# Performance work log

Hardware: AMD Instinct MI355X
Metric: run time of the kernel (lower is better)

The kernel has to match this reference:

```python
import jax, jax.numpy as jnp
import numpy as np

TOP_K_PCT = 0.1
MAX_SHARP_TOKENS = 10
SMOOTHING = 0.1


def setup_inputs() -> dict:
    key = jax.random.key(0)
    logits = jax.random.normal(key, (2, 8, 2048, 2048), dtype=jnp.float32)
    return {"logits": logits, "dim": 3}


def reference(logits, dim):
    # Move the softmax axis to the end so lax.top_k / row-scatter apply.
    x = jnp.moveaxis(logits, dim, -1)
    N = x.shape[-1]
    k = min(MAX_SHARP_TOKENS, max(1, int(N * TOP_K_PCT)))

    vals, idx = jax.lax.top_k(x, k)            # [..., k], sorted descending
    topk_soft = jax.nn.softmax(vals, axis=-1)  # softmax over just the top-k values

    flat = x.reshape(-1, N)                    # [R, N]
    fidx = idx.reshape(-1, k)                  # [R, k]
    rows = jnp.arange(flat.shape[0])[:, None]

    # boolean mask of top-k positions
    mask = jnp.zeros(flat.shape, dtype=bool).at[rows, fidx].set(True)

    # softmax over the remaining (non-top-k) logits; top-k filled with dtype min
    neg_inf = jnp.finfo(flat.dtype).min
    remaining = jnp.where(mask, neg_inf, flat)
    rem_soft = jax.nn.softmax(remaining, axis=-1)
    rem_soft = jnp.where(mask, jnp.zeros((), flat.dtype), rem_soft)

    # scatter top-k softmax back, then blend
    final = jnp.zeros_like(flat).at[rows, fidx].set(topk_soft.reshape(-1, k))
    out = final * (1.0 - SMOOTHING) + rem_soft * SMOOTHING

    return jnp.moveaxis(out.reshape(x.shape), -1, dim)
```

## Files before the change

kernel.cpp:

```cpp
#include <hip/hip_runtime.h>
#include <math.h>

#define ROW_N 2048
#define KSEL 10
#define WCAP 64

typedef float f32x4 __attribute__((ext_vector_type(4)));
typedef unsigned long long u64;

__global__ __launch_bounds__(256) void topk_softmax_kernel(
    const float* __restrict__ in, float* __restrict__ out)
{
    const int lane = threadIdx.x & 63;
    const int wave = threadIdx.x >> 6;
    const size_t baseA = ((size_t)blockIdx.x * 4 + wave) * 2 * ROW_N;
    const size_t baseB = baseA + ROW_N;

    __shared__ u64 s_cand[4][WCAP];

    const f32x4* pA = reinterpret_cast<const f32x4*>(in + baseA);
    const f32x4* pB = reinterpret_cast<const f32x4*>(in + baseB);
    f32x4 VA[8], VB[8];
    #pragma unroll
    for (int j = 0; j < 8; ++j) { VA[j] = pA[j * 64 + lane];
                                  VB[j] = pB[j * 64 + lane]; }

    const float K = 1.4426950408889634f;
    float a1 = -INFINITY, a2 = -INFINITY, a3 = -INFINITY, tA0 = 0.f;
    float b1 = -INFINITY, b2 = -INFINITY, b3 = -INFINITY, tB0 = 0.f;
    #pragma unroll
    for (int j = 0; j < 8; ++j)
        #pragma unroll
        for (int c = 0; c < 4; ++c) {
            float xA = VA[j][c];
            a3 = fmaxf(fminf(xA, a2), a3);
            a2 = fmaxf(fminf(xA, a1), a2);
            a1 = fmaxf(xA, a1);
            tA0 += exp2f(xA * K);
            float xB = VB[j][c];
            b3 = fmaxf(fminf(xB, b2), b3);
            b2 = fmaxf(fminf(xB, b1), b2);
            b1 = fmaxf(xB, b1);
            tB0 += exp2f(xB * K);
        }

    float vmA = a1, vmB = b1;
    #pragma unroll
    for (int off = 32; off > 0; off >>= 1) {
        vmA = fmaxf(vmA, __shfl_xor(vmA, off));  tA0 += __shfl_xor(tA0, off);
        vmB = fmaxf(vmB, __shfl_xor(vmB, off));  tB0 += __shfl_xor(tB0, off);
    }

    auto ord = [](float x) {
        uint32_t u = __float_as_uint(x);
        return u ^ ((uint32_t)((int32_t)u >> 31) | 0x80000000u);
    };
    const uint32_t oa1 = ord(a1), oa2 = ord(a2);
    const uint32_t ob1 = ord(b1), ob2 = ord(b2);

    uint32_t kA = 0, kB = 0;
    #pragma unroll
    for (int b = 31; b >= 0; --b) {
        uint32_t tA = kA | (1u << b), tB = kB | (1u << b);
        int cA = __popcll(__ballot(oa1 >= tA)) + __popcll(__ballot(oa2 >= tA));
        int cB = __popcll(__ballot(ob1 >= tB)) + __popcll(__ballot(ob2 >= tB));
        if (cA >= KSEL) kA = tA;
        if (cB >= KSEL) kB = tB;
    }
    auto unord = [](uint32_t o) {
        return __uint_as_float(o ^ ((o & 0x80000000u) ? 0x80000000u
                                                      : 0xFFFFFFFFu));
    };
    const float kfA = unord(kA), kfB = unord(kB);

    int cA10 = __popcll(__ballot(oa1 >= kA)) + __popcll(__ballot(oa2 >= kA));
    int cB10 = __popcll(__ballot(ob1 >= kB)) + __popcll(__ballot(ob2 >= kB));
    const bool fastA = (cA10 == KSEL) && (__ballot(a3 >= kfA) == 0ULL);
    const bool fastB = (cB10 == KSEL) && (__ballot(b3 >= kfB) == 0ULL);

    const float c0A = -vmA * K, c0B = -vmB * K;
    const float totA = tA0 * exp2f(c0A);
    const float totB = tB0 * exp2f(c0B);

    float eA = ((a1 >= kfA) ? exp2f(fmaf(a1, K, c0A)) : 0.f) +
               ((a2 >= kfA) ? exp2f(fmaf(a2, K, c0A)) : 0.f);
    float eB = ((b1 >= kfB) ? exp2f(fmaf(b1, K, c0B)) : 0.f) +
               ((b2 >= kfB) ? exp2f(fmaf(b2, K, c0B)) : 0.f);
    #pragma unroll
    for (int off = 32; off > 0; off >>= 1) {
        eA += __shfl_xor(eA, off);
        eB += __shfl_xor(eB, off);
    }

    const int low0 = 2047 - lane * 4;

    auto emit = [&](f32x4 (&V)[8], size_t base, float kf, float c0v,
                    float tot, float ssum, bool fast) {
        f32x4* o4 = reinterpret_cast<f32x4*>(out + base);
        if (fast) {
            const float aa = 0.9f / ssum;
            const float bb = 0.1f / (tot - ssum);
            #pragma unroll
            for (int j = 0; j < 8; ++j) {
                f32x4 o;
                #pragma unroll
                for (int c = 0; c < 4; ++c) {
                    float x = V[j][c];
                    o[c] = exp2f(fmaf(x, K, c0v)) * ((x >= kf) ? aa : bb);
                }
                __builtin_nontemporal_store(o, o4 + j * 64 + lane);
            }
        } else {
            int C = 0;
            #pragma unroll
            for (int j = 0; j < 8; ++j)
                #pragma unroll
                for (int c = 0; c < 4; ++c) {
                    bool cond = V[j][c] >= kf;
                    u64 m = __ballot(cond);
                    if (cond) {
                        uint32_t u  = __float_as_uint(V[j][c]);
                        uint32_t ov = u ^ ((uint32_t)((int32_t)u >> 31) | 0x80000000u);
                        int pos = C + (int)__builtin_amdgcn_mbcnt_hi(
                                          (unsigned)(m >> 32),
                                          __builtin_amdgcn_mbcnt_lo((unsigned)m, 0u));
                        if (pos < WCAP)
                            s_cand[wave][pos] =
                                ((u64)ov << 16) | (unsigned)(low0 - (j * 256 + c));
                    }
                    C += __popcll(m);
                }
            if (C > WCAP) C = WCAP;
            u64 k0 = (lane < C) ? s_cand[wave][lane] : 0ULL;
            u64 kmin = 0ULL;
            #pragma unroll 1
            for (int b = 47; b >= 0; --b) {
                u64 trial = kmin | (1ULL << b);
                if (__popcll(__ballot(k0 >= trial)) >= KSEL) kmin = trial;
            }
            uint32_t ovk  = (uint32_t)(k0 >> 16);
            uint32_t bits = ovk ^ ((ovk & 0x80000000u) ? 0x80000000u : 0xFFFFFFFFu);
            float val = __uint_as_float(bits);
            bool win  = (k0 >= kmin) && (k0 != 0ULL);
            float ee  = win ? exp2f(fmaf(val, K, c0v)) : 0.f;
            float ss = ee;
            #pragma unroll
            for (int off = 32; off > 0; off >>= 1) ss += __shfl_xor(ss, off);
            const float aa = 0.9f / ss;
            const float bb = 0.1f / (tot - ss);
            #pragma unroll
            for (int j = 0; j < 8; ++j) {
                f32x4 o;
                #pragma unroll
                for (int c = 0; c < 4; ++c) {
                    float x = V[j][c];
                    uint32_t u  = __float_as_uint(x);
                    uint32_t ov = u ^ ((uint32_t)((int32_t)u >> 31) | 0x80000000u);
                    u64 key = ((u64)ov << 16) | (unsigned)(low0 - (j * 256 + c));
                    o[c] = exp2f(fmaf(x, K, c0v)) * ((key >= kmin) ? aa : bb);
                }
                __builtin_nontemporal_store(o, o4 + j * 64 + lane);
            }
        }
    };

    emit(VA, baseA, kfA, c0A, totA, eA, fastA);
    emit(VB, baseB, kfB, c0B, totB, eB, fastB);
}

extern "C" void kernel_launch(void* const* d_in, const int* in_sizes, int n_in,
                              void* d_out, int out_size, void* d_ws, size_t ws_size,
                              hipStream_t stream) {
    const float* logits = (const float*)d_in[0];
    float* out = (float*)d_out;
    const int rows = out_size / ROW_N;
    topk_softmax_kernel<<<dim3(rows / 8), dim3(256), 0, stream>>>(logits, out);
}
```

Baseline: 434.9 us.

## Prefetch four rows per wave and use radix-4 threshold search

Each wave now loads four rows up front into registers, with asm barriers that keep the loads issued early, and then processes them as two pairs. The loads for the second pair overlap the compute of the first, raising memory-level parallelism per wave. The bitwise threshold search now resolves two bits per step with three parallel ballot counts, halving the serial chain length. In exchange the kernel holds 128 VGPRs of row data per lane, which lowers occupancy, and launches half as many blocks.

```diff
diff --git a/kernel.cpp b/kernel.cpp
--- a/kernel.cpp
+++ b/kernel.cpp
@@ -8,94 +8,40 @@
 typedef float f32x4 __attribute__((ext_vector_type(4)));
 typedef unsigned long long u64;
 
+__device__ __forceinline__ uint32_t ordbits(float x) {
+    uint32_t u = __float_as_uint(x);
+    return u ^ ((uint32_t)((int32_t)u >> 31) | 0x80000000u);
+}
+__device__ __forceinline__ float unord(uint32_t o) {
+    return __uint_as_float(o ^ ((o & 0x80000000u) ? 0x80000000u : 0xFFFFFFFFu));
+}
+
 __global__ __launch_bounds__(256) void topk_softmax_kernel(
     const float* __restrict__ in, float* __restrict__ out)
 {
     const int lane = threadIdx.x & 63;
     const int wave = threadIdx.x >> 6;
-    const size_t baseA = ((size_t)blockIdx.x * 4 + wave) * 2 * ROW_N;
-    const size_t baseB = baseA + ROW_N;
+    const size_t row0 = ((size_t)blockIdx.x * 4 + wave) * 4;
 
     __shared__ u64 s_cand[4][WCAP];
 
-    const f32x4* pA = reinterpret_cast<const f32x4*>(in + baseA);
-    const f32x4* pB = reinterpret_cast<const f32x4*>(in + baseB);
-    f32x4 VA[8], VB[8];
+    const float K = 1.4426950408889634f;
+    const int low0 = 2047 - lane * 4;
+
+    f32x4 V[4][8];
     #pragma unroll
-    for (int j = 0; j < 8; ++j) { VA[j] = pA[j * 64 + lane];
-                                  VB[j] = pB[j * 64 + lane]; }
-
-    const float K = 1.4426950408889634f;
-    float a1 = -INFINITY, a2 = -INFINITY, a3 = -INFINITY, tA0 = 0.f;
-    float b1 = -INFINITY, b2 = -INFINITY, b3 = -INFINITY, tB0 = 0.f;
-    #pragma unroll
-    for (int j = 0; j < 8; ++j)
+    for (int p = 0; p < 4; ++p) {
+        const f32x4* src = reinterpret_cast<const f32x4*>(in + (row0 + p) * ROW_N);
         #pragma unroll
-        for (int c = 0; c < 4; ++c) {
-            float xA = VA[j][c];
-            a3 = fmaxf(fminf(xA, a2), a3);
-            a2 = fmaxf(fminf(xA, a1), a2);
-            a1 = fmaxf(xA, a1);
-            tA0 += exp2f(xA * K);
-            float xB = VB[j][c];
-            b3 = fmaxf(fminf(xB, b2), b3);
-            b2 = fmaxf(fminf(xB, b1), b2);
-            b1 = fmaxf(xB, b1);
-            tB0 += exp2f(xB * K);
+        for (int j = 0; j < 8; ++j) {
+            V[p][j] = src[j * 64 + lane];
+            asm volatile("" : "+v"(V[p][j][0]), "+v"(V[p][j][1]),
+                              "+v"(V[p][j][2]), "+v"(V[p][j][3]));
         }
-
-    float vmA = a1, vmB = b1;
-    #pragma unroll
-    for (int off = 32; off > 0; off >>= 1) {
-        vmA = fmaxf(vmA, __shfl_xor(vmA, off));  tA0 += __shfl_xor(tA0, off);
-        vmB = fmaxf(vmB, __shfl_xor(vmB, off));  tB0 += __shfl_xor(tB0, off);
     }
 
-    auto ord = [](float x) {
-        uint32_t u = __float_as_uint(x);
-        return u ^ ((uint32_t)((int32_t)u >> 31) | 0x80000000u);
-    };
-    const uint32_t oa1 = ord(a1), oa2 = ord(a2);
-    const uint32_t ob1 = ord(b1), ob2 = ord(b2);
-
-    uint32_t kA = 0, kB = 0;
-    #pragma unroll
-    for (int b = 31; b >= 0; --b) {
-        uint32_t tA = kA | (1u << b), tB = kB | (1u << b);
-        int cA = __popcll(__ballot(oa1 >= tA)) + __popcll(__ballot(oa2 >= tA));
-        int cB = __popcll(__ballot(ob1 >= tB)) + __popcll(__ballot(ob2 >= tB));
-        if (cA >= KSEL) kA = tA;
-        if (cB >= KSEL) kB = tB;
-    }
-    auto unord = [](uint32_t o) {
-        return __uint_as_float(o ^ ((o & 0x80000000u) ? 0x80000000u
-                                                      : 0xFFFFFFFFu));
-    };
-    const float kfA = unord(kA), kfB = unord(kB);
-
-    int cA10 = __popcll(__ballot(oa1 >= kA)) + __popcll(__ballot(oa2 >= kA));
-    int cB10 = __popcll(__ballot(ob1 >= kB)) + __popcll(__ballot(ob2 >= kB));
-    const bool fastA = (cA10 == KSEL) && (__ballot(a3 >= kfA) == 0ULL);
-    const bool fastB = (cB10 == KSEL) && (__ballot(b3 >= kfB) == 0ULL);
-
-    const float c0A = -vmA * K, c0B = -vmB * K;
-    const float totA = tA0 * exp2f(c0A);
-    const float totB = tB0 * exp2f(c0B);
-
-    float eA = ((a1 >= kfA) ? exp2f(fmaf(a1, K, c0A)) : 0.f) +
-               ((a2 >= kfA) ? exp2f(fmaf(a2, K, c0A)) : 0.f);
-    float eB = ((b1 >= kfB) ? exp2f(fmaf(b1, K, c0B)) : 0.f) +
-               ((b2 >= kfB) ? exp2f(fmaf(b2, K, c0B)) : 0.f);
-    #pragma unroll
-    for (int off = 32; off > 0; off >>= 1) {
-        eA += __shfl_xor(eA, off);
-        eB += __shfl_xor(eB, off);
-    }
-
-    const int low0 = 2047 - lane * 4;
-
-    auto emit = [&](f32x4 (&V)[8], size_t base, float kf, float c0v,
-                    float tot, float ssum, bool fast) {
+    auto emitRow = [&](f32x4 (&Vr)[8], size_t base, float kf, float c0v,
+                       float tot, float ssum, bool fast) {
         f32x4* o4 = reinterpret_cast<f32x4*>(out + base);
         if (fast) {
             const float aa = 0.9f / ssum;
@@ -105,7 +51,7 @@
                 f32x4 o;
                 #pragma unroll
                 for (int c = 0; c < 4; ++c) {
-                    float x = V[j][c];
+                    float x = Vr[j][c];
                     o[c] = exp2f(fmaf(x, K, c0v)) * ((x >= kf) ? aa : bb);
                 }
                 __builtin_nontemporal_store(o, o4 + j * 64 + lane);
@@ -116,11 +62,10 @@
             for (int j = 0; j < 8; ++j)
                 #pragma unroll
                 for (int c = 0; c < 4; ++c) {
-                    bool cond = V[j][c] >= kf;
+                    bool cond = Vr[j][c] >= kf;
                     u64 m = __ballot(cond);
                     if (cond) {
-                        uint32_t u  = __float_as_uint(V[j][c]);
-                        uint32_t ov = u ^ ((uint32_t)((int32_t)u >> 31) | 0x80000000u);
+                        uint32_t ov = ordbits(Vr[j][c]);
                         int pos = C + (int)__builtin_amdgcn_mbcnt_hi(
                                           (unsigned)(m >> 32),
                                           __builtin_amdgcn_mbcnt_lo((unsigned)m, 0u));
@@ -139,8 +84,7 @@
                 if (__popcll(__ballot(k0 >= trial)) >= KSEL) kmin = trial;
             }
             uint32_t ovk  = (uint32_t)(k0 >> 16);
-            uint32_t bits = ovk ^ ((ovk & 0x80000000u) ? 0x80000000u : 0xFFFFFFFFu);
-            float val = __uint_as_float(bits);
+            float val = unord(ovk);
             bool win  = (k0 >= kmin) && (k0 != 0ULL);
             float ee  = win ? exp2f(fmaf(val, K, c0v)) : 0.f;
             float ss = ee;
@@ -153,10 +97,9 @@
                 f32x4 o;
                 #pragma unroll
                 for (int c = 0; c < 4; ++c) {
-                    float x = V[j][c];
-                    uint32_t u  = __float_as_uint(x);
-                    uint32_t ov = u ^ ((uint32_t)((int32_t)u >> 31) | 0x80000000u);
-                    u64 key = ((u64)ov << 16) | (unsigned)(low0 - (j * 256 + c));
+                    float x = Vr[j][c];
+                    u64 key = ((u64)ordbits(x) << 16) |
+                              (unsigned)(low0 - (j * 256 + c));
                     o[c] = exp2f(fmaf(x, K, c0v)) * ((key >= kmin) ? aa : bb);
                 }
                 __builtin_nontemporal_store(o, o4 + j * 64 + lane);
@@ -164,8 +107,77 @@
         }
     };
 
-    emit(VA, baseA, kfA, c0A, totA, eA, fastA);
-    emit(VB, baseB, kfB, c0B, totB, eB, fastB);
+    auto processPair = [&](f32x4 (&VA)[8], f32x4 (&VB)[8],
+                           size_t baseA, size_t baseB) {
+        float a1 = -INFINITY, a2 = -INFINITY, a3 = -INFINITY, tA0 = 0.f;
+        float b1 = -INFINITY, b2 = -INFINITY, b3 = -INFINITY, tB0 = 0.f;
+        #pragma unroll
+        for (int j = 0; j < 8; ++j)
+            #pragma unroll
+            for (int c = 0; c < 4; ++c) {
+                float xA = VA[j][c];
+                a3 = fmaxf(fminf(xA, a2), a3);
+                a2 = fmaxf(fminf(xA, a1), a2);
+                a1 = fmaxf(xA, a1);
+                tA0 += exp2f(xA * K);
+                float xB = VB[j][c];
+                b3 = fmaxf(fminf(xB, b2), b3);
+                b2 = fmaxf(fminf(xB, b1), b2);
+                b1 = fmaxf(xB, b1);
+                tB0 += exp2f(xB * K);
+            }
+
+        float vmA = a1, vmB = b1;
+        #pragma unroll
+        for (int off = 32; off > 0; off >>= 1) {
+            vmA = fmaxf(vmA, __shfl_xor(vmA, off)); tA0 += __shfl_xor(tA0, off);
+            vmB = fmaxf(vmB, __shfl_xor(vmB, off)); tB0 += __shfl_xor(tB0, off);
+        }
+
+        const uint32_t oa1 = ordbits(a1), oa2 = ordbits(a2);
+        const uint32_t ob1 = ordbits(b1), ob2 = ordbits(b2);
+        auto cntA = [&](uint32_t t) {
+            return __popcll(__ballot(oa1 >= t)) + __popcll(__ballot(oa2 >= t));
+        };
+        auto cntB = [&](uint32_t t) {
+            return __popcll(__ballot(ob1 >= t)) + __popcll(__ballot(ob2 >= t));
+        };
+
+        uint32_t kA = 0, kB = 0;
+        #pragma unroll
+        for (int b = 30; b >= 0; b -= 2) {
+            uint32_t A3 = kA | (3u << b), A2 = kA | (2u << b), A1 = kA | (1u << b);
+            uint32_t B3 = kB | (3u << b), B2 = kB | (2u << b), B1 = kB | (1u << b);
+            int cA3 = cntA(A3), cA2 = cntA(A2), cA1 = cntA(A1);
+            int cB3 = cntB(B3), cB2 = cntB(B2), cB1 = cntB(B1);
+            kA = (cA3 >= KSEL) ? A3 : (cA2 >= KSEL) ? A2 : (cA1 >= KSEL) ? A1 : kA;
+            kB = (cB3 >= KSEL) ? B3 : (cB2 >= KSEL) ? B2 : (cB1 >= KSEL) ? B1 : kB;
+        }
+        const float kfA = unord(kA), kfB = unord(kB);
+
+        const bool fastA = (cntA(kA) == KSEL) && (__ballot(a3 >= kfA) == 0ULL);
+        const bool fastB = (cntB(kB) == KSEL) && (__ballot(b3 >= kfB) == 0ULL);
+
+        const float c0A = -vmA * K, c0B = -vmB * K;
+        const float totA = tA0 * exp2f(c0A);
+        const float totB = tB0 * exp2f(c0B);
+
+        float eA = ((a1 >= kfA) ? exp2f(fmaf(a1, K, c0A)) : 0.f) +
+                   ((a2 >= kfA) ? exp2f(fmaf(a2, K, c0A)) : 0.f);
+        float eB = ((b1 >= kfB) ? exp2f(fmaf(b1, K, c0B)) : 0.f) +
+                   ((b2 >= kfB) ? exp2f(fmaf(b2, K, c0B)) : 0.f);
+        #pragma unroll
+        for (int off = 32; off > 0; off >>= 1) {
+            eA += __shfl_xor(eA, off);
+            eB += __shfl_xor(eB, off);
+        }
+
+        emitRow(VA, baseA, kfA, c0A, totA, eA, fastA);
+        emitRow(VB, baseB, kfB, c0B, totB, eB, fastB);
+    };
+
+    processPair(V[0], V[1], (row0 + 0) * ROW_N, (row0 + 1) * ROW_N);
+    processPair(V[2], V[3], (row0 + 2) * ROW_N, (row0 + 3) * ROW_N);
 }
 
 extern "C" void kernel_launch(void* const* d_in, const int* in_sizes, int n_in,
@@ -174,5 +186,5 @@
     const float* logits = (const float*)d_in[0];
     float* out = (float*)d_out;
     const int rows = out_size / ROW_N;
-    topk_softmax_kernel<<<dim3(rows / 8), dim3(256), 0, stream>>>(logits, out);
+    topk_softmax_kernel<<<dim3(rows / 16), dim3(256), 0, stream>>>(logits, out);
 }
```

After: 577.3 us. +32.7%, slower.
